# Optimization experiments

Measured on AMD Instinct MI355X. Metric: run time of the kernel, lower is better.

The kernel has to match this reference:

```python
import jax, jax.numpy as jnp
import numpy as np

C = 256   # channel
NH = 8    # n_heads
NP = 8    # n_points (n_levels = 1)
HD = C // NH


def conv1x1(x, W, b):
    # x: [B,C,H,W], W: [Cout,Cin] -> 1x1 conv == channel-mixing GEMM
    return jnp.einsum('bchw,oc->bohw', x, W) + b[None, :, None, None]


def linear(x, W, b):
    # x: [B,Q,Cin], W: [Cout,Cin] (torch nn.Linear layout)
    return jnp.einsum('bqc,oc->bqo', x, W) + b


def msda(value, loc, attn_w, H, Wd):
    # Multi-scale deformable attention core (single level).
    # value:  [B,Q,NH,HD]  (Q = H*Wd)
    # loc:    [B,Q,NH,NP,2] normalized sampling locations in [0,1] (x,y)
    # attn_w: [B,Q,NH,NP]  softmax weights
    B, Q = value.shape[0], value.shape[1]
    v = jnp.transpose(value, (0, 2, 1, 3))  # [B,NH,HW,HD]
    # grid_sample(align_corners=False): pixel coord = loc*size - 0.5
    ix = loc[..., 0] * Wd - 0.5
    iy = loc[..., 1] * H - 0.5
    x0 = jnp.floor(ix)
    y0 = jnp.floor(iy)

    def gather(xi, yi, wgt):
        valid = ((xi >= 0) & (xi < Wd) & (yi >= 0) & (yi < H)).astype(wgt.dtype)
        xc = jnp.clip(xi, 0, Wd - 1).astype(jnp.int32)
        yc = jnp.clip(yi, 0, H - 1).astype(jnp.int32)
        idx = yc * Wd + xc                                  # [B,Q,NH,NP]
        idx = jnp.transpose(idx, (0, 2, 1, 3)).reshape(B, NH, Q * NP)
        s = jnp.take_along_axis(v, idx[..., None], axis=2)  # [B,NH,Q*NP,HD]
        s = s.reshape(B, NH, Q, NP, HD)
        w = jnp.transpose(wgt * valid, (0, 2, 1, 3))[..., None]
        return s * w

    acc = (gather(x0, y0, (x0 + 1 - ix) * (y0 + 1 - iy))
           + gather(x0 + 1, y0, (ix - x0) * (y0 + 1 - iy))
           + gather(x0, y0 + 1, (x0 + 1 - ix) * (iy - y0))
           + gather(x0 + 1, y0 + 1, (ix - x0) * (iy - y0)))
    aw = jnp.transpose(attn_w, (0, 2, 1, 3))[..., None]      # [B,NH,Q,NP,1]
    out = (acc * aw).sum(axis=3)                             # [B,NH,Q,HD]
    return jnp.transpose(out, (0, 2, 1, 3)).reshape(B, Q, C)


def setup_inputs() -> dict:
    key = jax.random.key(0)
    ks = jax.random.split(key, 24)
    B, H, W = 2, 128, 128

    def w(k, shape, s=0.02):
        return jax.random.normal(k, shape, jnp.float32) * s

    d = {
        'xt': jax.random.normal(ks[0], (B, C, H, W), jnp.float32),
        'xt_1': jax.random.normal(ks[1], (B, C, H, W), jnp.float32),
        'W_in1': w(ks[2], (C, C)), 'b_in1': jnp.zeros((C,), jnp.float32),
        'W_in2': w(ks[3], (C, C)), 'b_in2': jnp.zeros((C,), jnp.float32),
        'Wv': w(ks[4], (C, C)), 'bv': jnp.zeros((C,), jnp.float32),
        'Ws': w(ks[5], (NH * NP * 2, C)), 'bs_off': w(ks[6], (NH * NP * 2,), 1.0),
        'Wa': w(ks[7], (NH * NP, C)), 'ba': jnp.zeros((NH * NP,), jnp.float32),
        'Wo': w(ks[8], (C, C)), 'bo': jnp.zeros((C,), jnp.float32),
        'Wt1': w(ks[9], (C, C)), 'bt1': jnp.zeros((C,), jnp.float32),
        'Wt2': w(ks[10], (C, C)), 'bt2': jnp.zeros((C,), jnp.float32),
        'Wout': w(ks[11], (C, C)), 'bout': jnp.zeros((C,), jnp.float32),
    }
    return d


def reference(xt, xt_1, W_in1, b_in1, W_in2, b_in2, Wv, bv, Ws, bs_off,
              Wa, ba, Wo, bo, Wt1, bt1, Wt2, bt2, Wout, bout):
    x1 = conv1x1(xt, W_in1, b_in1)
    x2 = conv1x1(xt_1, W_in2, b_in2)
    B, _, H, Wd = x1.shape
    Q = H * Wd
    q = jnp.transpose(x1, (0, 2, 3, 1)).reshape(B, Q, C)       # queries
    vflat = jnp.transpose(x2, (0, 2, 3, 1)).reshape(B, Q, C)   # values

    value = linear(vflat, Wv, bv).reshape(B, Q, NH, HD)
    offsets = linear(q, Ws, bs_off).reshape(B, Q, NH, NP, 2)
    attn = jax.nn.softmax(linear(q, Wa, ba).reshape(B, Q, NH, NP), axis=-1)

    # reference points at pixel centers, normalized (x,y)
    gy, gx = jnp.meshgrid(jnp.arange(H), jnp.arange(Wd), indexing='ij')
    ref = jnp.stack([(gx.reshape(-1) + 0.5) / Wd,
                     (gy.reshape(-1) + 0.5) / H], axis=-1).astype(jnp.float32)
    norm = jnp.array([Wd, H], jnp.float32)
    loc = ref[None, :, None, None, :] + offsets / norm          # [B,Q,NH,NP,2]

    out = msda(value, loc, attn, H, Wd)                         # [B,Q,C]
    xt_star = jnp.transpose(linear(out, Wo, bo), (0, 2, 1)).reshape(B, C, H, Wd)

    tg = conv1x1(jax.nn.relu(conv1x1(x1 * xt_star, Wt1, bt1)), Wt2, bt2)
    return jax.nn.relu(conv1x1(x1 + tg, Wout, bout))
```

## Files before the change

### kernel.cpp

```cpp
#include <hip/hip_runtime.h>
#include <math.h>


#define PIX 16384
#define BATCH 2
#define CH 256

typedef short bf16x8 __attribute__((ext_vector_type(8)));
typedef float f32x4 __attribute__((ext_vector_type(4)));

__device__ __forceinline__ ushort f2bf(float f) {
  union { float f; unsigned u; } v; v.f = f;
  unsigned u = v.u;
  unsigned r = u + 0x7fffu + ((u >> 16) & 1u);
  return (ushort)(r >> 16);
}
__device__ __forceinline__ float bfl(unsigned u) {
  union { unsigned u; float f; } v; v.u = u << 16; return v.f;
}
__device__ __forceinline__ float bfh(unsigned u) {
  union { unsigned u; float f; } v; v.u = u & 0xffff0000u; return v.f;
}
__device__ __forceinline__ unsigned fuse_u32(unsigned a, unsigned b, bool mul) {
  float rl = mul ? bfl(a) * bfl(b) : bfl(a) + bfl(b);
  float rh = mul ? bfh(a) * bfh(b) : bfh(a) + bfh(b);
  return (unsigned)f2bf(rl) | ((unsigned)f2bf(rh) << 16);
}

__global__ __launch_bounds__(256) void wprep_k(
    const float* __restrict__ W_in1, const float* __restrict__ Wo,
    const float* __restrict__ Wt1, const float* __restrict__ Wt2,
    const float* __restrict__ Wout, const float* __restrict__ Ws,
    const float* __restrict__ Wa, const float* __restrict__ bs_off,
    const float* __restrict__ ba, ushort* __restrict__ wb,
    float* __restrict__ bsa)
{
  const int blk = blockIdx.x, k = threadIdx.x;
  if (blk >= 1472) {
    if (k < 128) bsa[k] = bs_off[k];
    else if (k < 192) bsa[k] = ba[k - 128];
    return;
  }
  const float* src;
  if (blk < 256) src = W_in1 + (size_t)blk * 256;
  else if (blk < 512) src = Wo + (size_t)(blk - 256) * 256;
  else if (blk < 768) src = Wt1 + (size_t)(blk - 512) * 256;
  else if (blk < 1024) src = Wt2 + (size_t)(blk - 768) * 256;
  else if (blk < 1280) src = Wout + (size_t)(blk - 1024) * 256;
  else if (blk < 1408) src = Ws + (size_t)(blk - 1280) * 256;
  else src = Wa + (size_t)(blk - 1408) * 256;
  wb[(size_t)blk * 256 + k] = f2bf(src[k]);
}

__global__ __launch_bounds__(256) void wvcomp_k(
    const float* __restrict__ Wv, const float* __restrict__ W_in2,
    const float* __restrict__ b_in2, const float* __restrict__ bv,
    ushort* __restrict__ Wvp, float* __restrict__ bvp)
{
  const int o = blockIdx.x, k = threadIdx.x;
  float acc = 0.f;
  #pragma unroll 8
  for (int c = 0; c < 256; ++c)
    acc += Wv[(size_t)o * 256 + c] * W_in2[(size_t)c * 256 + k];
  Wvp[(size_t)o * 256 + k] = f2bf(acc);
  __shared__ float red[256];
  red[k] = Wv[(size_t)o * 256 + k] * b_in2[k];
  __syncthreads();
  for (int s = 128; s > 0; s >>= 1) {
    if (k < s) red[k] += red[k + s];
    __syncthreads();
  }
  if (k == 0) bvp[o] = red[0] + bv[o];
}

__global__ __launch_bounds__(256) void tconv_k(const float* __restrict__ in,
                                               ushort* __restrict__ out)
{
  __shared__ float t[32][33];
  const int tid = threadIdx.x;
  const int b = blockIdx.z;
  const int p0 = blockIdx.x * 32, c0 = blockIdx.y * 32;
  const int tx = tid & 31, ty = tid >> 5;
  const float* inb = in + (size_t)b * CH * PIX;
  #pragma unroll
  for (int i = 0; i < 4; ++i)
    t[ty + i * 8][tx] = inb[(size_t)(c0 + ty + i * 8) * PIX + p0 + tx];
  __syncthreads();
  const int cx = (tid & 15) * 2, py = tid >> 4;
  ushort* outb = out + (size_t)b * PIX * CH;
  #pragma unroll
  for (int i = 0; i < 2; ++i) {
    int pl = py + i * 16;
    unsigned lo = f2bf(t[cx][pl]);
    unsigned hi = f2bf(t[cx + 1][pl]);
    *(unsigned*)(outb + (size_t)(p0 + pl) * CH + c0 + cx) = lo | (hi << 16);
  }
}

template<int FUSE, bool RELU, int OMODE>
__global__ __launch_bounds__(256, 3) void gemm2_k(
    const ushort* __restrict__ in, const ushort* __restrict__ in2,
    const ushort* __restrict__ Wb, const float* __restrict__ bias,
    void* __restrict__ out, int ldo, size_t obstride)
{
  __shared__ __align__(16) char smem[49152];
  const int tid = threadIdx.x;
  const int b = blockIdx.z;
  const int p0 = blockIdx.x * 128;
  const int o0 = blockIdx.y * 64;

  const ushort* inb = in + (size_t)b * PIX * CH;

  const int srow = tid >> 3, sseg = tid & 7;
  const int ssw = (srow & 7);
  const ushort* xsrc = inb + (size_t)(p0 + srow) * CH + sseg * 8;
  const ushort* x2src = (FUSE != 0)
      ? in2 + (size_t)b * PIX * CH + (size_t)(p0 + srow) * CH + sseg * 8
      : (const ushort*)nullptr;
  const ushort* wsrc = Wb + (size_t)(o0 + srow) * CH + sseg * 8;

  const int l = tid & 63, wv = tid >> 6;
  const int lr = l & 15, g4 = l >> 4;

  f32x4 acc[2][4];
  #pragma unroll
  for (int i = 0; i < 2; ++i)
    #pragma unroll
    for (int j = 0; j < 4; ++j) acc[i][j] = (f32x4){0.f, 0.f, 0.f, 0.f};

  uint4 xr[4], x2r[4], wr[2];

#define LOADT(kb)                                                              \
  {                                                                            \
    _Pragma("unroll")                                                          \
    for (int r = 0; r < 4; ++r)                                                \
      xr[r] = *(const uint4*)(xsrc + (kb) + (size_t)r * 32 * CH);              \
    if (FUSE != 0) {                                                           \
      _Pragma("unroll")                                                        \
      for (int r = 0; r < 4; ++r)                                              \
        x2r[r] = *(const uint4*)(x2src + (kb) + (size_t)r * 32 * CH);          \
    }                                                                          \
    _Pragma("unroll")                                                          \
    for (int r = 0; r < 2; ++r)                                                \
      wr[r] = *(const uint4*)(wsrc + (kb) + (size_t)r * 32 * CH);              \
  }

#define WRITET(buf)                                                            \
  {                                                                            \
    _Pragma("unroll")                                                          \
    for (int r = 0; r < 4; ++r) {                                              \
      uint4 v = xr[r];                                                         \
      if (FUSE != 0) {                                                         \
        unsigned* pa = (unsigned*)&v;                                          \
        const unsigned* pb = (const unsigned*)&x2r[r];                         \
        _Pragma("unroll")                                                      \
        for (int w = 0; w < 4; ++w) pa[w] = fuse_u32(pa[w], pb[w], FUSE == 1); \
      }                                                                        \
      *(uint4*)(smem + (buf) * 16384 + (srow + r * 32) * 128 +                 \
                ((sseg ^ ssw) * 16)) = v;                                      \
    }                                                                          \
    _Pragma("unroll")                                                          \
    for (int r = 0; r < 2; ++r)                                                \
      *(uint4*)(smem + 32768 + (buf) * 8192 + (srow + r * 32) * 128 +          \
                ((sseg ^ ssw) * 16)) = wr[r];                                  \
  }

  LOADT(0)
  WRITET(0)
  __syncthreads();

  for (int t = 0; t < 4; ++t) {
    if (t < 3) LOADT((t + 1) * 64)
    const char* XB = smem + (t & 1) * 16384;
    const char* WB = smem + 32768 + (t & 1) * 8192;
    bf16x8 af[2][2], bfr[4][2];
    #pragma unroll
    for (int fm = 0; fm < 2; ++fm) {
      const int p = wv * 32 + fm * 16 + lr;
      #pragma unroll
      for (int kh = 0; kh < 2; ++kh)
        af[fm][kh] = *(const bf16x8*)(XB + p * 128 + (((kh * 4 + g4) ^ (p & 7)) * 16));
    }
    #pragma unroll
    for (int fn = 0; fn < 4; ++fn) {
      const int o = fn * 16 + lr;
      #pragma unroll
      for (int kh = 0; kh < 2; ++kh)
        bfr[fn][kh] = *(const bf16x8*)(WB + o * 128 + (((kh * 4 + g4) ^ (o & 7)) * 16));
    }
    #pragma unroll
    for (int fm = 0; fm < 2; ++fm)
      #pragma unroll
      for (int fn = 0; fn < 4; ++fn) {
        acc[fm][fn] = __builtin_amdgcn_mfma_f32_16x16x32_bf16(af[fm][0], bfr[fn][0], acc[fm][fn], 0, 0, 0);
        acc[fm][fn] = __builtin_amdgcn_mfma_f32_16x16x32_bf16(af[fm][1], bfr[fn][1], acc[fm][fn], 0, 0, 0);
      }
    if (t < 3) WRITET((t + 1) & 1)
    __syncthreads();
  }
#undef LOADT
#undef WRITET

  float bvv[4];
  #pragma unroll
  for (int fn = 0; fn < 4; ++fn) bvv[fn] = bias[o0 + fn * 16 + lr];

  if (OMODE == 1) {
    float* El2 = (float*)smem;
    #pragma unroll
    for (int fm = 0; fm < 2; ++fm)
      #pragma unroll
      for (int fn = 0; fn < 4; ++fn) {
        float4 v;
        v.x = acc[fm][fn][0] + bvv[fn]; v.y = acc[fm][fn][1] + bvv[fn];
        v.z = acc[fm][fn][2] + bvv[fn]; v.w = acc[fm][fn][3] + bvv[fn];
        if (RELU) {
          v.x = fmaxf(v.x, 0.f); v.y = fmaxf(v.y, 0.f);
          v.z = fmaxf(v.z, 0.f); v.w = fmaxf(v.w, 0.f);
        }
        *(float4*)&El2[(size_t)(fn * 16 + lr) * 132 + wv * 32 + fm * 16 + g4 * 4] = v;
      }
    __syncthreads();
    float* outb = (float*)out + (size_t)b * obstride;
    const int og = tid >> 5, seg = tid & 31;
    #pragma unroll
    for (int r = 0; r < 8; ++r) {
      const int orow = og + r * 8;
      float4 v = *(float4*)(smem + orow * 528 + seg * 16);
      *(float4*)(outb + (size_t)(o0 + orow) * ldo + p0 + seg * 4) = v;
    }
  } else if (OMODE == 0) {
    ushort* El = (ushort*)smem;
    #pragma unroll
    for (int fm = 0; fm < 2; ++fm)
      #pragma unroll
      for (int fn = 0; fn < 4; ++fn)
        #pragma unroll
        for (int r = 0; r < 4; ++r) {
          const int p = wv * 32 + fm * 16 + g4 * 4 + r;
          float v = acc[fm][fn][r] + bvv[fn];
          if (RELU) v = fmaxf(v, 0.f);
          El[p * 72 + fn * 16 + lr] = f2bf(v);
        }
    __syncthreads();
    ushort* outb = (ushort*)out + (size_t)b * obstride;
    const int rg = tid >> 3, seg = tid & 7;
    #pragma unroll
    for (int r = 0; r < 4; ++r) {
      const int row = rg + r * 32;
      uint4 v = *(uint4*)(smem + row * 144 + seg * 16);
      *(uint4*)(outb + (size_t)(p0 + row) * ldo + o0 + seg * 8) = v;
    }
  } else {
    float* El = (float*)smem;
    #pragma unroll
    for (int fm = 0; fm < 2; ++fm)
      #pragma unroll
      for (int fn = 0; fn < 4; ++fn)
        #pragma unroll
        for (int r = 0; r < 4; ++r) {
          const int p = wv * 32 + fm * 16 + g4 * 4 + r;
          float v = acc[fm][fn][r] + bvv[fn];
          if (RELU) v = fmaxf(v, 0.f);
          El[p * 68 + fn * 16 + lr] = v;
        }
    __syncthreads();
    float* outb = (float*)out + (size_t)b * obstride;
    const int rg = tid >> 4, seg = tid & 15;
    #pragma unroll
    for (int r = 0; r < 8; ++r) {
      const int row = rg + r * 16;
      float4 v = *(float4*)(smem + row * 272 + seg * 16);
      *(float4*)(outb + (size_t)(p0 + row) * ldo + o0 + seg * 4) = v;
    }
  }
}

__global__ __launch_bounds__(256) void msda_k(
    const ushort* __restrict__ value, const float* __restrict__ sa,
    ushort* __restrict__ out)
{
  const int t = blockIdx.x * 256 + threadIdx.x;
  const int dh = t & 1;
  const int h = (t >> 1) & 7;
  const int pg = t >> 4;
  const int b = pg >> 14;
  const int p = pg & (PIX - 1);
  const int px = p & 127, py = p >> 7;

  const ushort* vb = value + (size_t)b * PIX * CH;
  const float* sp = sa + (size_t)pg * 192;

  float4 la = *(const float4*)(sp + 128 + h * 8);
  float4 lb = *(const float4*)(sp + 128 + h * 8 + 4);
  float lg[8] = {la.x, la.y, la.z, la.w, lb.x, lb.y, lb.z, lb.w};
  float m = lg[0];
  #pragma unroll
  for (int i = 1; i < 8; ++i) m = fmaxf(m, lg[i]);
  float s = 0.f;
  #pragma unroll
  for (int i = 0; i < 8; ++i) { lg[i] = __expf(lg[i] - m); s += lg[i]; }
  const float inv = 1.f / s;

  float of[16];
  #pragma unroll
  for (int j = 0; j < 4; ++j)
    *(float4*)&of[j * 4] = *(const float4*)(sp + h * 16 + j * 4);

  float acc[16];
  #pragma unroll
  for (int i = 0; i < 16; ++i) acc[i] = 0.f;

  #pragma unroll
  for (int pt = 0; pt < 8; ++pt) {
    const float ox = of[2 * pt], oy = of[2 * pt + 1];
    const float aw = lg[pt] * inv;
    const float ix = px + ox, iy = py + oy;
    const float xf = floorf(ix), yf = floorf(iy);
    const float fx = ix - xf, fy = iy - yf;
    const int x0 = (int)xf, y0 = (int)yf;
    #pragma unroll
    for (int cr = 0; cr < 4; ++cr) {
      const int dx = cr & 1, dy = cr >> 1;
      const int xx = x0 + dx, yy = y0 + dy;
      const float wx = dx ? fx : (1.f - fx);
      const float wy = dy ? fy : (1.f - fy);
      const bool valid = ((unsigned)xx < 128u) & ((unsigned)yy < 128u);
      float w = valid ? (wx * wy * aw) : 0.f;
      const int xc = min(max(xx, 0), 127), yc = min(max(yy, 0), 127);
      const ushort* vr = vb + ((size_t)(yc * 128 + xc) * CH + h * 32 + dh * 16);
      uint4 q0 = *(const uint4*)vr;
      uint4 q1 = *(const uint4*)(vr + 8);
      const unsigned* qw0 = (const unsigned*)&q0;
      const unsigned* qw1 = (const unsigned*)&q1;
      #pragma unroll
      for (int ww = 0; ww < 4; ++ww) {
        acc[2 * ww + 0] = fmaf(w, bfl(qw0[ww]), acc[2 * ww + 0]);
        acc[2 * ww + 1] = fmaf(w, bfh(qw0[ww]), acc[2 * ww + 1]);
        acc[8 + 2 * ww + 0] = fmaf(w, bfl(qw1[ww]), acc[8 + 2 * ww + 0]);
        acc[8 + 2 * ww + 1] = fmaf(w, bfh(qw1[ww]), acc[8 + 2 * ww + 1]);
      }
    }
  }
  unsigned r[8];
  #pragma unroll
  for (int k = 0; k < 8; ++k)
    r[k] = (unsigned)f2bf(acc[2 * k]) | ((unsigned)f2bf(acc[2 * k + 1]) << 16);
  ushort* dst = out + (size_t)pg * CH + h * 32 + dh * 16;
  *(uint4*)dst = *(uint4*)&r[0];
  *(uint4*)(dst + 8) = *(uint4*)&r[4];
}

extern "C" void kernel_launch(void* const* d_in, const int* in_sizes, int n_in,
                              void* d_out, int out_size, void* d_ws, size_t ws_size,
                              hipStream_t stream)
{
  const float* xt     = (const float*)d_in[0];
  const float* xt_1   = (const float*)d_in[1];
  const float* W_in1  = (const float*)d_in[2];
  const float* b_in1  = (const float*)d_in[3];
  const float* W_in2  = (const float*)d_in[4];
  const float* b_in2  = (const float*)d_in[5];
  const float* Wv     = (const float*)d_in[6];
  const float* bv     = (const float*)d_in[7];
  const float* Ws     = (const float*)d_in[8];
  const float* bs_off = (const float*)d_in[9];
  const float* Wa     = (const float*)d_in[10];
  const float* ba     = (const float*)d_in[11];
  const float* Wo     = (const float*)d_in[12];
  const float* bo     = (const float*)d_in[13];
  const float* Wt1    = (const float*)d_in[14];
  const float* bt1    = (const float*)d_in[15];
  const float* Wt2    = (const float*)d_in[16];
  const float* bt2    = (const float*)d_in[17];
  const float* Wout   = (const float*)d_in[18];
  const float* bout   = (const float*)d_in[19];

  char* ws = (char*)d_ws;
  const size_t SLOT = (size_t)BATCH * PIX * CH * 2;
  const size_t SAB  = (size_t)BATCH * PIX * 192 * 4;
  ushort* s0 = (ushort*)(ws + 0 * SLOT);
  ushort* s1 = (ushort*)(ws + 1 * SLOT);
  ushort* s2 = (ushort*)(ws + 2 * SLOT);
  ushort* s3 = (ushort*)(ws + 3 * SLOT);
  ushort* s4 = (ushort*)(ws + 4 * SLOT);
  float*  sa = (float*)(ws + 5 * SLOT);
  char* wbase = ws + 5 * SLOT + SAB;
  ushort* wb  = (ushort*)wbase;
  ushort* wvp = (ushort*)(wbase + (size_t)1472 * 256 * 2);
  float* bsa  = (float*)(wbase + (size_t)1472 * 256 * 2 + (size_t)256 * 256 * 2);
  float* bvp  = bsa + 192;

  ushort* wb_in1 = wb;
  ushort* wb_o   = wb + 65536;
  ushort* wb_t1  = wb + 131072;
  ushort* wb_t2  = wb + 196608;
  ushort* wb_out = wb + 262144;
  ushort* wb_sa  = wb + 327680;

  dim3 blk(256);
  dim3 gT(PIX / 32, CH / 32, BATCH);
  dim3 gF(PIX / 128, 4, BATCH);
  dim3 gS(PIX / 128, 3, BATCH);
  const size_t OBS = (size_t)PIX * CH;

  wprep_k<<<1473, blk, 0, stream>>>(W_in1, Wo, Wt1, Wt2, Wout, Ws, Wa, bs_off, ba, wb, bsa);
  wvcomp_k<<<256, blk, 0, stream>>>(Wv, W_in2, b_in2, bv, wvp, bvp);
  tconv_k<<<gT, blk, 0, stream>>>(xt, s0);
  tconv_k<<<gT, blk, 0, stream>>>(xt_1, s1);

  gemm2_k<0, false, 0><<<gF, blk, 0, stream>>>(s0, nullptr, wb_in1, b_in1, s2, CH, OBS);
  gemm2_k<0, false, 0><<<gF, blk, 0, stream>>>(s1, nullptr, wvp, bvp, s3, CH, OBS);
  gemm2_k<0, false, 2><<<gS, blk, 0, stream>>>(s2, nullptr, wb_sa, bsa, sa, 192, (size_t)PIX * 192);
  msda_k<<<dim3((BATCH * PIX * 16) / 256), blk, 0, stream>>>(s3, sa, s4);
  gemm2_k<0, false, 0><<<gF, blk, 0, stream>>>(s4, nullptr, wb_o, bo, s0, CH, OBS);
  gemm2_k<1, true , 0><<<gF, blk, 0, stream>>>(s0, s2, wb_t1, bt1, s1, CH, OBS);
  gemm2_k<0, false, 0><<<gF, blk, 0, stream>>>(s1, nullptr, wb_t2, bt2, s3, CH, OBS);
  gemm2_k<2, true , 1><<<gF, blk, 0, stream>>>(s3, s2, wb_out, bout, d_out, PIX, (size_t)CH * PIX);
}
```

Before: 170.8 us.

## Stage GEMM tiles via direct global-to-LDS loads and merge transpose launches

```diff
diff --git a/kernel.cpp b/kernel.cpp
--- a/kernel.cpp
+++ b/kernel.cpp
@@ -8,6 +8,12 @@
 
 typedef short bf16x8 __attribute__((ext_vector_type(8)));
 typedef float f32x4 __attribute__((ext_vector_type(4)));
+
+typedef const __attribute__((address_space(1))) void* as1cv;
+typedef __attribute__((address_space(3))) void* as3v;
+__device__ __forceinline__ void gl_lds16(const void* g, void* l) {
+  __builtin_amdgcn_global_load_lds((as1cv)g, (as3v)l, 16, 0, 0);
+}
 
 __device__ __forceinline__ ushort f2bf(float f) {
   union { float f; unsigned u; } v; v.f = f;
@@ -73,12 +79,16 @@
   if (k == 0) bvp[o] = red[0] + bv[o];
 }
 
-__global__ __launch_bounds__(256) void tconv_k(const float* __restrict__ in,
-                                               ushort* __restrict__ out)
+__global__ __launch_bounds__(256) void tconv2_k(
+    const float* __restrict__ inA, const float* __restrict__ inB,
+    ushort* __restrict__ outA, ushort* __restrict__ outB)
 {
   __shared__ float t[32][33];
   const int tid = threadIdx.x;
-  const int b = blockIdx.z;
+  const int z = blockIdx.z;
+  const int b = z & 1;
+  const float* in = (z < 2) ? inA : inB;
+  ushort* out = (z < 2) ? outA : outB;
   const int p0 = blockIdx.x * 32, c0 = blockIdx.y * 32;
   const int tx = tid & 31, ty = tid >> 5;
   const float* inb = in + (size_t)b * CH * PIX;
@@ -113,11 +123,12 @@
 
   const int srow = tid >> 3, sseg = tid & 7;
   const int ssw = (srow & 7);
-  const ushort* xsrc = inb + (size_t)(p0 + srow) * CH + sseg * 8;
+  const int gseg = (FUSE == 0) ? (sseg ^ ssw) : sseg;
+  const ushort* xsrc = inb + (size_t)(p0 + srow) * CH + gseg * 8;
   const ushort* x2src = (FUSE != 0)
       ? in2 + (size_t)b * PIX * CH + (size_t)(p0 + srow) * CH + sseg * 8
       : (const ushort*)nullptr;
-  const ushort* wsrc = Wb + (size_t)(o0 + srow) * CH + sseg * 8;
+  const ushort* wsrc = Wb + (size_t)(o0 + srow) * CH + gseg * 8;
 
   const int l = tid & 63, wv = tid >> 6;
   const int lr = l & 15, g4 = l >> 4;
@@ -130,16 +141,26 @@
 
   uint4 xr[4], x2r[4], wr[2];
 
+#define STAGE_GLL(buf, kb)                                                     \
+  {                                                                            \
+    _Pragma("unroll")                                                          \
+    for (int r = 0; r < 4; ++r)                                                \
+      gl_lds16(xsrc + (kb) + (size_t)r * 32 * CH,                              \
+               smem + (buf) * 16384 + r * 4096 + tid * 16);                    \
+    _Pragma("unroll")                                                          \
+    for (int r = 0; r < 2; ++r)                                                \
+      gl_lds16(wsrc + (kb) + (size_t)r * 32 * CH,                              \
+               smem + 32768 + (buf) * 8192 + r * 4096 + tid * 16);             \
+  }
+
 #define LOADT(kb)                                                              \
   {                                                                            \
     _Pragma("unroll")                                                          \
     for (int r = 0; r < 4; ++r)                                                \
       xr[r] = *(const uint4*)(xsrc + (kb) + (size_t)r * 32 * CH);              \
-    if (FUSE != 0) {                                                           \
-      _Pragma("unroll")                                                        \
-      for (int r = 0; r < 4; ++r)                                              \
-        x2r[r] = *(const uint4*)(x2src + (kb) + (size_t)r * 32 * CH);          \
-    }                                                                          \
+    _Pragma("unroll")                                                          \
+    for (int r = 0; r < 4; ++r)                                                \
+      x2r[r] = *(const uint4*)(x2src + (kb) + (size_t)r * 32 * CH);            \
     _Pragma("unroll")                                                          \
     for (int r = 0; r < 2; ++r)                                                \
       wr[r] = *(const uint4*)(wsrc + (kb) + (size_t)r * 32 * CH);              \
@@ -150,12 +171,10 @@
     _Pragma("unroll")                                                          \
     for (int r = 0; r < 4; ++r) {                                              \
       uint4 v = xr[r];                                                         \
-      if (FUSE != 0) {                                                         \
-        unsigned* pa = (unsigned*)&v;                                          \
-        const unsigned* pb = (const unsigned*)&x2r[r];                         \
-        _Pragma("unroll")                                                      \
-        for (int w = 0; w < 4; ++w) pa[w] = fuse_u32(pa[w], pb[w], FUSE == 1); \
-      }                                                                        \
+      unsigned* pa = (unsigned*)&v;                                            \
+      const unsigned* pb = (const unsigned*)&x2r[r];                           \
+      _Pragma("unroll")                                                        \
+      for (int w = 0; w < 4; ++w) pa[w] = fuse_u32(pa[w], pb[w], FUSE == 1);   \
       *(uint4*)(smem + (buf) * 16384 + (srow + r * 32) * 128 +                 \
                 ((sseg ^ ssw) * 16)) = v;                                      \
     }                                                                          \
@@ -165,12 +184,15 @@
                 ((sseg ^ ssw) * 16)) = wr[r];                                  \
   }
 
-  LOADT(0)
-  WRITET(0)
+  if (FUSE == 0) { STAGE_GLL(0, 0) }
+  else           { LOADT(0) WRITET(0) }
   __syncthreads();
 
   for (int t = 0; t < 4; ++t) {
-    if (t < 3) LOADT((t + 1) * 64)
+    if (t < 3) {
+      if (FUSE == 0) { STAGE_GLL((t + 1) & 1, (t + 1) * 64) }
+      else           { LOADT((t + 1) * 64) }
+    }
     const char* XB = smem + (t & 1) * 16384;
     const char* WB = smem + 32768 + (t & 1) * 8192;
     bf16x8 af[2][2], bfr[4][2];
@@ -195,9 +217,10 @@
         acc[fm][fn] = __builtin_amdgcn_mfma_f32_16x16x32_bf16(af[fm][0], bfr[fn][0], acc[fm][fn], 0, 0, 0);
         acc[fm][fn] = __builtin_amdgcn_mfma_f32_16x16x32_bf16(af[fm][1], bfr[fn][1], acc[fm][fn], 0, 0, 0);
       }
-    if (t < 3) WRITET((t + 1) & 1)
+    if (t < 3 && FUSE != 0) { WRITET((t + 1) & 1) }
     __syncthreads();
   }
+#undef STAGE_GLL
 #undef LOADT
 #undef WRITET
 
@@ -399,15 +422,14 @@
   ushort* wb_sa  = wb + 327680;
 
   dim3 blk(256);
-  dim3 gT(PIX / 32, CH / 32, BATCH);
+  dim3 gT(PIX / 32, CH / 32, 2 * BATCH);
   dim3 gF(PIX / 128, 4, BATCH);
   dim3 gS(PIX / 128, 3, BATCH);
   const size_t OBS = (size_t)PIX * CH;
 
   wprep_k<<<1473, blk, 0, stream>>>(W_in1, Wo, Wt1, Wt2, Wout, Ws, Wa, bs_off, ba, wb, bsa);
   wvcomp_k<<<256, blk, 0, stream>>>(Wv, W_in2, b_in2, bv, wvp, bvp);
-  tconv_k<<<gT, blk, 0, stream>>>(xt, s0);
-  tconv_k<<<gT, blk, 0, stream>>>(xt_1, s1);
+  tconv2_k<<<gT, blk, 0, stream>>>(xt, xt_1, s0, s1);
 
   gemm2_k<0, false, 0><<<gF, blk, 0, stream>>>(s0, nullptr, wb_in1, b_in1, s2, CH, OBS);
   gemm2_k<0, false, 0><<<gF, blk, 0, stream>>>(s1, nullptr, wvp, bvp, s3, CH, OBS);
```

Result: faster. 164.9 us (-3.4%).
